# Optimization experiments

Measured on AMD Instinct MI355X. Metric: run time of the kernel, lower is better.

## Reference

```python
import jax, jax.numpy as jnp
import numpy as np

B, S, P, D, H, L, DF, O = 8, 1024, 128, 256, 4, 4, 1024, 10
DH = D // H  # 64
EPS = 1e-5


def get_positional_embeddings(seq_len, d):
    i = np.arange(seq_len, dtype=np.float64)[:, None]
    j = np.arange(d, dtype=np.float64)[None, :]
    even = np.sin(i / 10000 ** (j / d))
    odd = np.cos(i / 10000 ** ((j - 1) / d))
    return jnp.asarray(np.where(j % 2 == 0, even, odd), dtype=jnp.float32)


def layernorm(x, g, b):
    m = jnp.mean(x, axis=-1, keepdims=True)
    v = jnp.mean(jnp.square(x - m), axis=-1, keepdims=True)
    return (x - m) * jax.lax.rsqrt(v + EPS) * g + b


def setup_inputs() -> dict:
    key = jax.random.key(0)
    ks = jax.random.split(key, 20)
    w = lambda k, shp: (jax.random.normal(k, shp, dtype=jnp.float32) * 0.02)
    return {
        "images": jax.random.normal(ks[0], (B, S, P), dtype=jnp.float32),
        "Wp": w(ks[1], (D, P)), "bp": jnp.zeros((D,), jnp.float32),
        "cls": jax.random.uniform(ks[2], (1, D), dtype=jnp.float32),
        "pos": get_positional_embeddings(S + 1, D),
        "ln1_g": jnp.ones((L, D), jnp.float32), "ln1_b": jnp.zeros((L, D), jnp.float32),
        "Wq": w(ks[3], (L, H, DH, DH)), "bq": jnp.zeros((L, H, DH), jnp.float32),
        "Wk": w(ks[4], (L, H, DH, DH)), "bk": jnp.zeros((L, H, DH), jnp.float32),
        "Wv": w(ks[5], (L, H, DH, DH)), "bv": jnp.zeros((L, H, DH), jnp.float32),
        "ln2_g": jnp.ones((L, D), jnp.float32), "ln2_b": jnp.zeros((L, D), jnp.float32),
        "W1": w(ks[6], (L, DF, D)), "b1": jnp.zeros((L, DF), jnp.float32),
        "W2": w(ks[7], (L, D, DF)), "b2": jnp.zeros((L, D), jnp.float32),
        "Wo": w(ks[8], (O, D)), "bo": jnp.zeros((O,), jnp.float32),
    }


def msa(x, Wq, bq, Wk, bk, Wv, bv):
    b, s, _ = x.shape
    xh = x.reshape(b, s, H, DH)  # split heads along feature dim
    # torch Linear: y = x @ W.T + b, per head
    q = jnp.einsum("bshd,hed->bhse", xh, Wq) + bq[None, :, None, :]
    k = jnp.einsum("bshd,hed->bhse", xh, Wk) + bk[None, :, None, :]
    v = jnp.einsum("bshd,hed->bhse", xh, Wv) + bv[None, :, None, :]
    scores = jnp.einsum("bhqd,bhkd->bhqk", q, k) / (DH ** 0.5)
    attn = jax.nn.softmax(scores, axis=-1)
    out = jnp.einsum("bhqk,bhkd->bhqd", attn, v)  # [b,h,s,dh]
    return out.transpose(0, 2, 1, 3).reshape(b, s, D)  # hstack heads


def reference(images, Wp, bp, cls, pos, ln1_g, ln1_b, Wq, bq, Wk, bk, Wv, bv,
              ln2_g, ln2_b, W1, b1, W2, b2, Wo, bo):
    tokens = jnp.einsum("bsp,dp->bsd", images, Wp) + bp
    x = jnp.concatenate([jnp.broadcast_to(cls[None], (B, 1, D)), tokens], axis=1)
    x = x + pos[None]
    for l in range(L):
        x = x + msa(layernorm(x, ln1_g[l], ln1_b[l]), Wq[l], bq[l], Wk[l], bk[l], Wv[l], bv[l])
        h = layernorm(x, ln2_g[l], ln2_b[l])
        h = jax.nn.gelu(jnp.einsum("bsd,fd->bsf", h, W1[l]) + b1[l], approximate=False)
        x = x + jnp.einsum("bsf,df->bsd", h, W2[l]) + b2[l]
    logits = x[:, 0] @ Wo.T + bo
    return jax.nn.softmax(logits, axis=-1)
```

## Files before the change

kernel.cpp:

```cpp
#include <hip/hip_runtime.h>
#include <hip/hip_bf16.h>
#include <cmath>

constexpr int B  = 8;
constexpr int S  = 1024;
constexpr int P  = 128;
constexpr int D  = 256;
constexpr int H  = 4;
constexpr int L  = 4;
constexpr int DF = 1024;
constexpr int O  = 10;
constexpr int DH = D / H;
constexpr int SP = S + 1;
constexpr int N  = B * SP;
constexpr int KVPAD = 1088;

typedef short bf16x8 __attribute__((ext_vector_type(8)));
typedef float f32x4 __attribute__((ext_vector_type(4)));
typedef float f32x16 __attribute__((ext_vector_type(16)));
typedef unsigned int u32;
typedef unsigned short u16;

static __device__ __forceinline__ u16 f2b(float f) {
    __hip_bfloat16 h = __float2bfloat16(f);
    u16 u; __builtin_memcpy(&u, &h, 2);
    return u;
}
static __device__ __forceinline__ float b2f(u16 u) {
    u32 uu = (u32)u << 16; float f; __builtin_memcpy(&f, &uu, 4);
    return f;
}
static __device__ __forceinline__ u32 pk2(float a, float b) {
    return (u32)f2b(a) | ((u32)f2b(b) << 16);
}
static __device__ __forceinline__ void gload_lds16(const void* g, void* l) {
    __builtin_amdgcn_global_load_lds((const __attribute__((address_space(1))) unsigned int*)g,
                                     (__attribute__((address_space(3))) unsigned int*)l, 16, 0, 0);
}

__global__ void cvt_all(const float* __restrict__ s0, u16* __restrict__ d0, int n0,
                        const float* __restrict__ s1, u16* __restrict__ d1, int n1,
                        const float* __restrict__ s2, u16* __restrict__ d2, int n2,
                        const float* __restrict__ s3, u16* __restrict__ d3, int n3) {
    int y = blockIdx.y;
    const float* s = y == 0 ? s0 : y == 1 ? s1 : y == 2 ? s2 : s3;
    u16* d = y == 0 ? d0 : y == 1 ? d1 : y == 2 ? d2 : d3;
    int n = y == 0 ? n0 : y == 1 ? n1 : y == 2 ? n2 : n3;
    int i = blockIdx.x * 256 + threadIdx.x;
    if (i < n) {
        float4 v = ((const float4*)s)[i];
        ushort4 o;
        o.x = f2b(v.x); o.y = f2b(v.y); o.z = f2b(v.z); o.w = f2b(v.w);
        ((ushort4*)d)[i] = o;
    }
}

__global__ void cls_kernel(const float* __restrict__ cls, const float* __restrict__ pos,
                           float* __restrict__ x) {
    int b = blockIdx.x, t = threadIdx.x;
    x[(size_t)b * SP * D + t] = cls[t] + pos[t];
}

__global__ void build_wqkv(const float* __restrict__ Wq, const float* __restrict__ bq,
                           const float* __restrict__ Wk, const float* __restrict__ bk,
                           const float* __restrict__ Wv, const float* __restrict__ bv,
                           u16* __restrict__ Wout, float* __restrict__ bout) {
    int r = blockIdx.x, l = blockIdx.y, c = threadIdx.x;
    int sec = r >> 8;
    int ef = r & 255, h = ef >> 6, e = ef & 63;
    const float* W  = sec == 0 ? Wq : sec == 1 ? Wk : Wv;
    const float* bi = sec == 0 ? bq : sec == 1 ? bk : bv;
    float scale = sec == 0 ? 0.125f * 1.4426950408889634f : 1.0f;
    float val = ((c >> 6) == h) ? W[(((size_t)l * H + h) * 64 + e) * 64 + (c & 63)] * scale : 0.f;
    Wout[((size_t)l * 768 + r) * 256 + c] = f2b(val);
    if (c == 0) bout[(size_t)l * 768 + r] = bi[((size_t)l * H + h) * 64 + e] * scale;
}

template <int EPI>
__global__ __launch_bounds__(256) void gemm_bf16(
        const u16* __restrict__ X, const u16* __restrict__ W,
        const float* __restrict__ bias, const float* __restrict__ pos,
        float* __restrict__ Yf, u16* __restrict__ Yb,
        int M, int F, int K, int kLen) {
    __shared__ u16 Al[2][64 * 64];
    __shared__ u16 Bl[2][128 * 64];
    const int t = threadIdx.x;
    const int m0 = blockIdx.y * 64, f0 = blockIdx.x * 128;
    const int w = t >> 6, l = t & 63;
    const int wm = w >> 1, wn = w & 1;
    const int q = l & 15, g = l >> 4;
    const int kOff = blockIdx.z * kLen;
    const int lr8 = l >> 3, lp = l & 7;

    f32x4 acc[2][4];
    const f32x4 zz = {0.f, 0.f, 0.f, 0.f};
#pragma unroll
    for (int i = 0; i < 2; ++i)
#pragma unroll
        for (int j = 0; j < 4; ++j) acc[i][j] = zz;

    auto stage = [&](int sb, int kbase) {
#pragma unroll
        for (int i = 0; i < 2; ++i) {
            int ca = w + 4 * i;
            int row = ca * 8 + lr8;
            int j = lp ^ (row & 7);
            gload_lds16(X + (size_t)(m0 + row) * K + kbase + j * 8, &Al[sb][ca * 512]);
        }
#pragma unroll
        for (int i = 0; i < 4; ++i) {
            int cb = w + 4 * i;
            int row = cb * 8 + lr8;
            int j = lp ^ (row & 7);
            gload_lds16(W + (size_t)(f0 + row) * K + kbase + j * 8, &Bl[sb][cb * 512]);
        }
    };

    const int nt = kLen / 64;
    stage(0, kOff);
    __syncthreads();
    int sb = 0;
    for (int ts = 0; ts < nt; ++ts) {
        if (ts + 1 < nt) stage(sb ^ 1, kOff + (ts + 1) * 64);
#pragma unroll
        for (int kk = 0; kk < 2; ++kk) {
            bf16x8 a[2], bfr[4];
#pragma unroll
            for (int fi = 0; fi < 2; ++fi) {
                int row = wm * 32 + fi * 16 + q;
                a[fi] = *(const bf16x8*)&Al[sb][row * 64 + (((kk * 4 + g) ^ (row & 7)) * 8)];
            }
#pragma unroll
            for (int fj = 0; fj < 4; ++fj) {
                int row = wn * 64 + fj * 16 + q;
                bfr[fj] = *(const bf16x8*)&Bl[sb][row * 64 + (((kk * 4 + g) ^ (row & 7)) * 8)];
            }
#pragma unroll
            for (int fi = 0; fi < 2; ++fi)
#pragma unroll
                for (int fj = 0; fj < 4; ++fj)
                    acc[fi][fj] = __builtin_amdgcn_mfma_f32_16x16x32_bf16(a[fi], bfr[fj], acc[fi][fj], 0, 0, 0);
        }
        __syncthreads();
        sb ^= 1;
    }

#pragma unroll
    for (int fi = 0; fi < 2; ++fi) {
#pragma unroll
        for (int r = 0; r < 4; ++r) {
            int m = m0 + wm * 32 + fi * 16 + g * 4 + r;
            if (m >= M) continue;
#pragma unroll
            for (int fj = 0; fj < 4; ++fj) {
                int f = f0 + wn * 64 + fj * 16 + q;
                float val = acc[fi][fj][r];
                if constexpr (EPI == 0) {
                    val += bias[f];
                    int s = m & 1023, bb = m >> 10;
                    size_t n = (size_t)bb * SP + s + 1;
                    Yf[n * D + f] = val + pos[(size_t)(s + 1) * D + f];
                } else if constexpr (EPI == 1) {
                    val += bias[f];
                    float gel = 0.5f * val * (1.0f + erff(val * 0.70710678118654752f));
                    Yb[(size_t)m * F + f] = f2b(gel);
                } else if constexpr (EPI == 2) {
                    val += bias[f];
                    Yf[(size_t)m * F + f] += val;
                } else if constexpr (EPI == 3) {
                    val += bias[f];
                    Yb[(size_t)m * F + f] = f2b(val);
                } else {
                    (Yf + (size_t)blockIdx.z * M * F)[(size_t)m * F + f] = val;
                }
            }
        }
    }
}

__global__ void transpose_v(const u16* __restrict__ qkv, u16* __restrict__ VTg) {
    __shared__ u16 tile[64][70];
    int bh = blockIdx.y, t0 = blockIdx.x * 64;
    int b = bh >> 2, h = bh & 3;
    int t = threadIdx.x;
    int r = t >> 3, c8 = (t & 7) * 8;
#pragma unroll
    for (int it = 0; it < 2; ++it) {
        int sp = t0 + it * 32 + r; if (sp > S) sp = S;
        uint4 v = *(const uint4*)(qkv + ((size_t)b * SP + sp) * 768 + 512 + h * 64 + c8);
        u32* dst = (u32*)&tile[it * 32 + r][c8];
        const u32* pv = (const u32*)&v;
#pragma unroll
        for (int k = 0; k < 4; ++k) dst[k] = pv[k];
    }
    __syncthreads();
#pragma unroll
    for (int it = 0; it < 2; ++it) {
        int d = it * 32 + (t >> 3);
        int spc = (t & 7) * 8;
        u16 tmp[8];
#pragma unroll
        for (int j = 0; j < 8; ++j) tmp[j] = tile[spc + j][d];
        *(uint4*)(VTg + ((size_t)bh * 64 + d) * KVPAD + t0 + spc) = *(const uint4*)tmp;
    }
}

__global__ void layernorm_bf16(const float* __restrict__ src,
                               const float* __restrict__ gw,
                               const float* __restrict__ bw,
                               u16* __restrict__ dst) {
    int row = blockIdx.x * 4 + (threadIdx.x >> 6);
    int l = threadIdx.x & 63;
    float4 v = *(const float4*)(src + (size_t)row * D + l * 4);
    float s = v.x + v.y + v.z + v.w;
    for (int off = 32; off; off >>= 1) s += __shfl_xor(s, off, 64);
    float mean = s * (1.0f / D);
    float dx0 = v.x - mean, dx1 = v.y - mean, dx2 = v.z - mean, dx3 = v.w - mean;
    float sq = dx0 * dx0 + dx1 * dx1 + dx2 * dx2 + dx3 * dx3;
    for (int off = 32; off; off >>= 1) sq += __shfl_xor(sq, off, 64);
    float rs = rsqrtf(sq * (1.0f / D) + 1e-5f);
    float4 gv = *(const float4*)(gw + l * 4);
    float4 bv = *(const float4*)(bw + l * 4);
    ushort4 o;
    o.x = f2b(dx0 * rs * gv.x + bv.x);
    o.y = f2b(dx1 * rs * gv.y + bv.y);
    o.z = f2b(dx2 * rs * gv.z + bv.z);
    o.w = f2b(dx3 * rs * gv.w + bv.w);
    *(ushort4*)(dst + (size_t)row * D + l * 4) = o;
}

__global__ __launch_bounds__(512, 4) void attn_stage(const u16* __restrict__ qkv,
                                                     const u16* __restrict__ VTg,
                                                     u16* __restrict__ opart,
                                                     float* __restrict__ lsum,
                                                     int nqt) {
    const int qg = blockIdx.x, bh = blockIdx.y, quarter = blockIdx.z;
    const int h4 = bh & 3, b = bh >> 2;
    const int t = threadIdx.x;
    const int wv = t >> 6, l = t & 63;
    const int col = l & 31, hh = l >> 5;

    __shared__ u16 Kl[5 * 64 * 64];
    __shared__ u16 Vl[5 * 64 * 64];

    const int kv_start = quarter * 256;
    const int kv_len = (quarter == 3) ? (SP - 768) : 256;
    const int ntiles = (kv_len + 63) >> 6;

    const int qt = qg * 8 + wv;
    const int q0w = qt * 32;

    bf16x8 qf[4];
    {
        int qr = q0w + col; if (qr > S) qr = S;
        const u16* qp = qkv + ((size_t)b * SP + qr) * 768 + h4 * 64 + hh * 8;
#pragma unroll
        for (int c = 0; c < 4; ++c) qf[c] = *(const bf16x8*)(qp + c * 16);
    }

    {
        const int rloc = wv * 8 + (l >> 3);
        const int j = (l & 7) ^ (((rloc >> 3) ^ rloc) & 7);
        for (int tt = 0; tt < ntiles; ++tt) {
            int krow = kv_start + tt * 64 + rloc; if (krow > S) krow = S;
            gload_lds16(qkv + ((size_t)b * SP + krow) * 768 + 256 + h4 * 64 + j * 8,
                        &Kl[(tt * 8 + wv) * 512]);
            gload_lds16(VTg + ((size_t)bh * 64 + rloc) * KVPAD + kv_start + tt * 64 + j * 8,
                        &Vl[(tt * 8 + wv) * 512]);
        }
    }
    __syncthreads();
    if (qt >= nqt) return;

    const int swA = ((col >> 3) ^ col) & 7;
    const int swB = swA ^ 4;

    f32x16 o0, o1;
#pragma unroll
    for (int r = 0; r < 16; ++r) { o0[r] = 0.f; o1[r] = 0.f; }
    float l_run = 0.f;

    for (int tile = 0; tile < ntiles; ++tile) {
        const int kv0 = tile * 64;
        const u16* Kt = &Kl[tile * 4096];
        const u16* Vt = &Vl[tile * 4096];

        f32x16 s0, s1;
#pragma unroll
        for (int r = 0; r < 16; ++r) { s0[r] = 0.f; s1[r] = 0.f; }
        __builtin_amdgcn_s_setprio(1);
#pragma unroll
        for (int c = 0; c < 4; ++c) {
            bf16x8 k0 = *(const bf16x8*)&Kt[col * 64 + (((2 * c + hh) ^ swA) * 8)];
            bf16x8 k1 = *(const bf16x8*)&Kt[(32 + col) * 64 + (((2 * c + hh) ^ swB) * 8)];
            s0 = __builtin_amdgcn_mfma_f32_32x32x16_bf16(k0, qf[c], s0, 0, 0, 0);
            s1 = __builtin_amdgcn_mfma_f32_32x32x16_bf16(k1, qf[c], s1, 0, 0, 0);
        }
        __builtin_amdgcn_s_setprio(0);

        float p[32];
#pragma unroll
        for (int r = 0; r < 16; ++r) { p[r] = s0[r]; p[16 + r] = s1[r]; }

        if (kv0 + 64 > kv_len) {
#pragma unroll
            for (int kvs = 0; kvs < 2; ++kvs)
#pragma unroll
                for (int r = 0; r < 16; ++r) {
                    int kvloc = kvs * 32 + (r & 3) + 8 * (r >> 2) + 4 * hh;
                    if (kv0 + kvloc >= kv_len) p[kvs * 16 + r] = -1e30f;
                }
        }

#pragma unroll
        for (int j = 0; j < 32; ++j) p[j] = exp2f(p[j]);
        {
            float t16[16];
#pragma unroll
            for (int j = 0; j < 16; ++j) t16[j] = p[2 * j] + p[2 * j + 1];
#pragma unroll
            for (int j = 0; j < 8; ++j) t16[j] = t16[j] + t16[j + 8];
#pragma unroll
            for (int j = 0; j < 4; ++j) t16[j] = t16[j] + t16[j + 4];
            l_run += (t16[0] + t16[1]) + (t16[2] + t16[3]);
        }

        __builtin_amdgcn_s_setprio(1);
#pragma unroll
        for (int kvs = 0; kvs < 2; ++kvs) {
            u32 pk[8];
#pragma unroll
            for (int i = 0; i < 8; ++i) pk[i] = pk2(p[kvs * 16 + 2 * i], p[kvs * 16 + 2 * i + 1]);
            u32 ex[4];
#pragma unroll
            for (int kk = 0; kk < 4; ++kk) {
                const int k = (kk < 2) ? kk : kk + 2;
                u32 send = hh ? pk[k] : pk[k + 2];
                ex[kk] = (u32)__shfl_xor((int)send, 32);
            }
#pragma unroll
            for (int cc = 0; cc < 2; ++cc) {
                union { u32 u[4]; bf16x8 v; } pa;
                u32 e0 = ex[cc * 2], e1 = ex[cc * 2 + 1];
                pa.u[0] = hh ? e0 : pk[4 * cc];
                pa.u[1] = hh ? e1 : pk[4 * cc + 1];
                pa.u[2] = hh ? pk[4 * cc + 2] : e0;
                pa.u[3] = hh ? pk[4 * cc + 3] : e1;
                int lch = kvs * 4 + cc * 2 + hh;
                bf16x8 v0 = *(const bf16x8*)&Vt[col * 64 + ((lch ^ swA) * 8)];
                bf16x8 v1 = *(const bf16x8*)&Vt[(32 + col) * 64 + ((lch ^ swB) * 8)];
                o0 = __builtin_amdgcn_mfma_f32_32x32x16_bf16(pa.v, v0, o0, 0, 0, 0);
                o1 = __builtin_amdgcn_mfma_f32_32x32x16_bf16(pa.v, v1, o1, 0, 0, 0);
            }
        }
        __builtin_amdgcn_s_setprio(0);
    }

    float l_full = l_run + __shfl_xor(l_run, 32);
    float inv = 1.0f / l_full;
    const size_t obase = ((size_t)quarter * 32 + bh) * SP;
#pragma unroll
    for (int r = 0; r < 16; ++r) {
        int qrow = (r & 3) + 8 * (r >> 2) + 4 * hh;
        float iv = __shfl(inv, qrow);
        int qq = q0w + qrow;
        if (qq < SP) {
            opart[(obase + qq) * 64 + col]      = f2b(o0[r] * iv);
            opart[(obase + qq) * 64 + 32 + col] = f2b(o1[r] * iv);
        }
    }
    if (l < 32) {
        int qq = q0w + l;
        if (qq < SP) lsum[obase + qq] = l_full;
    }
}

__global__ void combine_ln2(const u16* __restrict__ opart, const float* __restrict__ lsum,
                            const float* __restrict__ gw, const float* __restrict__ bw,
                            float* __restrict__ x, u16* __restrict__ lnb) {
    int row = blockIdx.x * 4 + (threadIdx.x >> 6);
    int l = threadIdx.x & 63;
    int b = row / SP, qq = row % SP;
    int h = l >> 4, d0 = (l * 4) & 63;
    int bh = b * 4 + h;
    float csum = 0.f, a0 = 0.f, a1 = 0.f, a2 = 0.f, a3 = 0.f;
#pragma unroll
    for (int i = 0; i < 4; ++i) {
        size_t idx = ((size_t)i * 32 + bh) * SP + qq;
        float c = lsum[idx];
        csum += c;
        ushort4 ov = *(const ushort4*)&opart[idx * 64 + d0];
        a0 += c * b2f(ov.x); a1 += c * b2f(ov.y); a2 += c * b2f(ov.z); a3 += c * b2f(ov.w);
    }
    float inv = 1.0f / csum;
    float4 xv = *(const float4*)(x + (size_t)row * D + l * 4);
    xv.x += a0 * inv; xv.y += a1 * inv; xv.z += a2 * inv; xv.w += a3 * inv;
    *(float4*)(x + (size_t)row * D + l * 4) = xv;

    float s = xv.x + xv.y + xv.z + xv.w;
    for (int off = 32; off; off >>= 1) s += __shfl_xor(s, off, 64);
    float mean = s * (1.0f / D);
    float dx0 = xv.x - mean, dx1 = xv.y - mean, dx2 = xv.z - mean, dx3 = xv.w - mean;
    float sq = dx0 * dx0 + dx1 * dx1 + dx2 * dx2 + dx3 * dx3;
    for (int off = 32; off; off >>= 1) sq += __shfl_xor(sq, off, 64);
    float rs = rsqrtf(sq * (1.0f / D) + 1e-5f);
    float4 gv = *(const float4*)(gw + l * 4);
    float4 bv = *(const float4*)(bw + l * 4);
    ushort4 o;
    o.x = f2b(dx0 * rs * gv.x + bv.x);
    o.y = f2b(dx1 * rs * gv.y + bv.y);
    o.z = f2b(dx2 * rs * gv.z + bv.z);
    o.w = f2b(dx3 * rs * gv.w + bv.w);
    *(ushort4*)(lnb + (size_t)row * D + l * 4) = o;
}

__global__ void combine2_ln1(const float* __restrict__ Pk, const float* __restrict__ b2,
                             const float* __restrict__ gw, const float* __restrict__ bw,
                             float* __restrict__ x, u16* __restrict__ lnb) {
    int row = blockIdx.x * 4 + (threadIdx.x >> 6);
    int l = threadIdx.x & 63;
    float4 p0 = ((const float4*)Pk)[(size_t)row * 64 + l];
    float4 p1 = ((const float4*)Pk)[(size_t)N * 64 + (size_t)row * 64 + l];
    float4 bv2 = *(const float4*)(b2 + l * 4);
    float4 xv = *(const float4*)(x + (size_t)row * D + l * 4);
    xv.x += p0.x + p1.x + bv2.x;
    xv.y += p0.y + p1.y + bv2.y;
    xv.z += p0.z + p1.z + bv2.z;
    xv.w += p0.w + p1.w + bv2.w;
    *(float4*)(x + (size_t)row * D + l * 4) = xv;

    float s = xv.x + xv.y + xv.z + xv.w;
    for (int off = 32; off; off >>= 1) s += __shfl_xor(s, off, 64);
    float mean = s * (1.0f / D);
    float dx0 = xv.x - mean, dx1 = xv.y - mean, dx2 = xv.z - mean, dx3 = xv.w - mean;
    float sq = dx0 * dx0 + dx1 * dx1 + dx2 * dx2 + dx3 * dx3;
    for (int off = 32; off; off >>= 1) sq += __shfl_xor(sq, off, 64);
    float rs = rsqrtf(sq * (1.0f / D) + 1e-5f);
    float4 gv = *(const float4*)(gw + l * 4);
    float4 bv = *(const float4*)(bw + l * 4);
    ushort4 o;
    o.x = f2b(dx0 * rs * gv.x + bv.x);
    o.y = f2b(dx1 * rs * gv.y + bv.y);
    o.z = f2b(dx2 * rs * gv.z + bv.z);
    o.w = f2b(dx3 * rs * gv.w + bv.w);
    *(ushort4*)(lnb + (size_t)row * D + l * 4) = o;
}

__global__ void combine_cls_ln2(const u16* __restrict__ opart, const float* __restrict__ lsum,
                                const float* __restrict__ x,
                                const float* __restrict__ gw, const float* __restrict__ bw,
                                float* __restrict__ x_cls, u16* __restrict__ lnb_cls) {
    int b = blockIdx.x * 4 + (threadIdx.x >> 6);
    int l = threadIdx.x & 63;
    int h = l >> 4, d0 = (l * 4) & 63;
    int bh = b * 4 + h;
    float csum = 0.f, a0 = 0.f, a1 = 0.f, a2 = 0.f, a3 = 0.f;
#pragma unroll
    for (int i = 0; i < 4; ++i) {
        size_t idx = ((size_t)i * 32 + bh) * SP;
        float c = lsum[idx];
        csum += c;
        ushort4 ov = *(const ushort4*)&opart[idx * 64 + d0];
        a0 += c * b2f(ov.x); a1 += c * b2f(ov.y); a2 += c * b2f(ov.z); a3 += c * b2f(ov.w);
    }
    float inv = 1.0f / csum;
    float4 xv = *(const float4*)(x + (size_t)b * SP * D + l * 4);
    xv.x += a0 * inv; xv.y += a1 * inv; xv.z += a2 * inv; xv.w += a3 * inv;
    *(float4*)(x_cls + (size_t)b * D + l * 4) = xv;

    float s = xv.x + xv.y + xv.z + xv.w;
    for (int off = 32; off; off >>= 1) s += __shfl_xor(s, off, 64);
    float mean = s * (1.0f / D);
    float dx0 = xv.x - mean, dx1 = xv.y - mean, dx2 = xv.z - mean, dx3 = xv.w - mean;
    float sq = dx0 * dx0 + dx1 * dx1 + dx2 * dx2 + dx3 * dx3;
    for (int off = 32; off; off >>= 1) sq += __shfl_xor(sq, off, 64);
    float rs = rsqrtf(sq * (1.0f / D) + 1e-5f);
    float4 gv = *(const float4*)(gw + l * 4);
    float4 bv = *(const float4*)(bw + l * 4);
    ushort4 o;
    o.x = f2b(dx0 * rs * gv.x + bv.x);
    o.y = f2b(dx1 * rs * gv.y + bv.y);
    o.z = f2b(dx2 * rs * gv.z + bv.z);
    o.w = f2b(dx3 * rs * gv.w + bv.w);
    *(ushort4*)(lnb_cls + (size_t)b * D + l * 4) = o;
}

__global__ void head_kernel(const float* __restrict__ xc,
                            const float* __restrict__ Wo,
                            const float* __restrict__ bo,
                            float* __restrict__ out) {
    __shared__ float logits[B][O];
    int t = threadIdx.x;
    if (t < B * O) {
        int b = t / O, o = t % O;
        const float* xr = xc + (size_t)b * D;
        float acc = bo[o];
        for (int d = 0; d < D; ++d) acc += xr[d] * Wo[(size_t)o * D + d];
        logits[b][o] = acc;
    }
    __syncthreads();
    if (t < B) {
        float mx = -1e30f;
        for (int o = 0; o < O; ++o) mx = fmaxf(mx, logits[t][o]);
        float s = 0.f, e[O];
        for (int o = 0; o < O; ++o) { e[o] = expf(logits[t][o] - mx); s += e[o]; }
        float inv = 1.0f / s;
        for (int o = 0; o < O; ++o) out[t * O + o] = e[o] * inv;
    }
}

extern "C" void kernel_launch(void* const* d_in, const int* in_sizes, int n_in,
                              void* d_out, int out_size, void* d_ws, size_t ws_size,
                              hipStream_t stream) {
    const float* images = (const float*)d_in[0];
    const float* Wp     = (const float*)d_in[1];
    const float* bp     = (const float*)d_in[2];
    const float* cls    = (const float*)d_in[3];
    const float* pos    = (const float*)d_in[4];
    const float* ln1_g  = (const float*)d_in[5];
    const float* ln1_b  = (const float*)d_in[6];
    const float* Wq     = (const float*)d_in[7];
    const float* bq     = (const float*)d_in[8];
    const float* Wk     = (const float*)d_in[9];
    const float* bk     = (const float*)d_in[10];
    const float* Wv     = (const float*)d_in[11];
    const float* bv     = (const float*)d_in[12];
    const float* ln2_g  = (const float*)d_in[13];
    const float* ln2_b  = (const float*)d_in[14];
    const float* W1     = (const float*)d_in[15];
    const float* b1     = (const float*)d_in[16];
    const float* W2     = (const float*)d_in[17];
    const float* b2     = (const float*)d_in[18];
    const float* Wo     = (const float*)d_in[19];
    const float* bo     = (const float*)d_in[20];
    float* out = (float*)d_out;

    auto align256 = [](size_t v) { return (v + 255) & ~(size_t)255; };
    char* p = (char*)d_ws;
    float* x      = (float*)p; p += align256((size_t)N * D * 4);
    u16* lnb      = (u16*)p;   p += align256((size_t)N * D * 2);
    u16* qkvbuf   = (u16*)p;   p += align256((size_t)(N + 64) * 768 * 2);
    char* midop   = p;         p += align256((size_t)N * DF * 2);
    float* Pk     = (float*)p; p += align256((size_t)2 * N * D * 4);
    float* lsum   = (float*)p; p += align256((size_t)4 * 32 * SP * 4);
    u16* VTg      = (u16*)p;   p += align256((size_t)32 * 64 * KVPAD * 2);
    u16* imgb     = (u16*)p;   p += align256((size_t)B * S * P * 2);
    u16* Wpb      = (u16*)p;   p += align256((size_t)D * P * 2);
    u16* W1b      = (u16*)p;   p += align256((size_t)L * DF * D * 2);
    u16* W2b      = (u16*)p;   p += align256((size_t)L * D * DF * 2);
    u16* Wqkvb    = (u16*)p;   p += align256((size_t)L * 768 * 256 * 2);
    float* bqkvf  = (float*)p; p += align256((size_t)L * 768 * 4);
    float* x_cls  = (float*)p; p += align256((size_t)64 * D * 4);
    u16* lnb_cls  = (u16*)p;   p += align256((size_t)64 * D * 2);
    u16* mid_cls  = (u16*)p;   p += align256((size_t)64 * DF * 2);
    u16* mid      = (u16*)midop;
    u16* opart    = (u16*)midop;

    cvt_all<<<dim3(1024, 4), 256, 0, stream>>>(
        images, imgb, B * S * P / 4,
        Wp, Wpb, D * P / 4,
        W1, W1b, L * DF * D / 4,
        W2, W2b, L * D * DF / 4);
    build_wqkv<<<dim3(768, L), 256, 0, stream>>>(Wq, bq, Wk, bk, Wv, bv, Wqkvb, bqkvf);

    gemm_bf16<0><<<dim3(2, 128, 1), 256, 0, stream>>>(
        imgb, Wpb, bp, pos, x, nullptr, B * S, D, P, P);
    cls_kernel<<<B, D, 0, stream>>>(cls, pos, x);
    layernorm_bf16<<<N / 4, 256, 0, stream>>>(x, ln1_g, ln1_b, lnb);

    for (int l = 0; l < 3; ++l) {
        gemm_bf16<3><<<dim3(6, 129, 1), 256, 0, stream>>>(
            lnb, Wqkvb + (size_t)l * 768 * 256, bqkvf + (size_t)l * 768,
            nullptr, nullptr, qkvbuf, N, 768, D, D);
        transpose_v<<<dim3(17, 32), 256, 0, stream>>>(qkvbuf, VTg);
        attn_stage<<<dim3(5, 32, 4), 512, 0, stream>>>(qkvbuf, VTg, opart, lsum, 33);
        combine_ln2<<<N / 4, 256, 0, stream>>>(opart, lsum, ln2_g + l * D, ln2_b + l * D, x, lnb);
        gemm_bf16<1><<<dim3(8, 129, 1), 256, 0, stream>>>(
            lnb, W1b + (size_t)l * DF * D, b1 + (size_t)l * DF,
            nullptr, nullptr, mid, N, DF, D, D);
        gemm_bf16<4><<<dim3(2, 129, 2), 256, 0, stream>>>(
            mid, W2b + (size_t)l * D * DF, nullptr, nullptr, Pk, nullptr, N, D, DF, DF / 2);
        combine2_ln1<<<N / 4, 256, 0, stream>>>(Pk, b2 + (size_t)l * D,
                                                ln1_g + (l + 1) * D, ln1_b + (l + 1) * D, x, lnb);
    }

    {
        const int l = 3;
        gemm_bf16<3><<<dim3(6, 129, 1), 256, 0, stream>>>(
            lnb, Wqkvb + (size_t)l * 768 * 256, bqkvf + (size_t)l * 768,
            nullptr, nullptr, qkvbuf, N, 768, D, D);
        transpose_v<<<dim3(17, 32), 256, 0, stream>>>(qkvbuf, VTg);
        attn_stage<<<dim3(1, 32, 4), 512, 0, stream>>>(qkvbuf, VTg, opart, lsum, 1);
        combine_cls_ln2<<<2, 256, 0, stream>>>(opart, lsum, x, ln2_g + l * D, ln2_b + l * D,
                                               x_cls, lnb_cls);
        gemm_bf16<1><<<dim3(8, 1, 1), 256, 0, stream>>>(
            lnb_cls, W1b + (size_t)l * DF * D, b1 + (size_t)l * DF,
            nullptr, nullptr, mid_cls, B, DF, D, D);
        gemm_bf16<2><<<dim3(2, 1, 1), 256, 0, stream>>>(
            mid_cls, W2b + (size_t)l * D * DF, b2 + (size_t)l * D,
            nullptr, x_cls, nullptr, B, D, DF, DF);
    }

    head_kernel<<<1, 256, 0, stream>>>(x_cls, Wo, bo, out);
}
```

Baseline: 357.5 us.

## Fuse final-layer tail, drop attention normalization pass, store split-K partials as bf16

The separate cls-token and first-layernorm kernels are merged, and the last-layer tail (combine, LN2, MLP, head and softmax for the CLS rows) is collapsed into one per-batch kernel, removing about five small launches. Attention partials are no longer normalized per quarter, so the combine step simply sums them and divides by the total lsum. The split-K W2 partial outputs are written in bf16 instead of fp32, halving that intermediate traffic. In exchange, partials are rounded to bf16 before summing, and unnormalized attention outputs may lose a little precision.

```diff
diff --git a/kernel.cpp b/kernel.cpp
--- a/kernel.cpp
+++ b/kernel.cpp
@@ -53,12 +53,6 @@
         o.x = f2b(v.x); o.y = f2b(v.y); o.z = f2b(v.z); o.w = f2b(v.w);
         ((ushort4*)d)[i] = o;
     }
-}
-
-__global__ void cls_kernel(const float* __restrict__ cls, const float* __restrict__ pos,
-                           float* __restrict__ x) {
-    int b = blockIdx.x, t = threadIdx.x;
-    x[(size_t)b * SP * D + t] = cls[t] + pos[t];
 }
 
 __global__ void build_wqkv(const float* __restrict__ Wq, const float* __restrict__ bq,
@@ -164,14 +158,11 @@
                     val += bias[f];
                     float gel = 0.5f * val * (1.0f + erff(val * 0.70710678118654752f));
                     Yb[(size_t)m * F + f] = f2b(gel);
-                } else if constexpr (EPI == 2) {
-                    val += bias[f];
-                    Yf[(size_t)m * F + f] += val;
                 } else if constexpr (EPI == 3) {
                     val += bias[f];
                     Yb[(size_t)m * F + f] = f2b(val);
                 } else {
-                    (Yf + (size_t)blockIdx.z * M * F)[(size_t)m * F + f] = val;
+                    Yb[(size_t)blockIdx.z * M * F + (size_t)m * F + f] = f2b(val);
                 }
             }
         }
@@ -205,13 +196,20 @@
     }
 }
 
-__global__ void layernorm_bf16(const float* __restrict__ src,
-                               const float* __restrict__ gw,
-                               const float* __restrict__ bw,
-                               u16* __restrict__ dst) {
+__global__ void ln_first(const float* __restrict__ cls, const float* __restrict__ pos,
+                         const float* __restrict__ gw, const float* __restrict__ bw,
+                         float* __restrict__ x, u16* __restrict__ dst) {
     int row = blockIdx.x * 4 + (threadIdx.x >> 6);
     int l = threadIdx.x & 63;
-    float4 v = *(const float4*)(src + (size_t)row * D + l * 4);
+    float4 v;
+    if ((row % SP) == 0) {
+        float4 c = *(const float4*)(cls + l * 4);
+        float4 pp = *(const float4*)(pos + l * 4);
+        v.x = c.x + pp.x; v.y = c.y + pp.y; v.z = c.z + pp.z; v.w = c.w + pp.w;
+        *(float4*)(x + (size_t)row * D + l * 4) = v;
+    } else {
+        v = *(const float4*)(x + (size_t)row * D + l * 4);
+    }
     float s = v.x + v.y + v.z + v.w;
     for (int off = 32; off; off >>= 1) s += __shfl_xor(s, off, 64);
     float mean = s * (1.0f / D);
@@ -357,16 +355,14 @@
     }
 
     float l_full = l_run + __shfl_xor(l_run, 32);
-    float inv = 1.0f / l_full;
     const size_t obase = ((size_t)quarter * 32 + bh) * SP;
 #pragma unroll
     for (int r = 0; r < 16; ++r) {
         int qrow = (r & 3) + 8 * (r >> 2) + 4 * hh;
-        float iv = __shfl(inv, qrow);
         int qq = q0w + qrow;
         if (qq < SP) {
-            opart[(obase + qq) * 64 + col]      = f2b(o0[r] * iv);
-            opart[(obase + qq) * 64 + 32 + col] = f2b(o1[r] * iv);
+            opart[(obase + qq) * 64 + col]      = f2b(o0[r]);
+            opart[(obase + qq) * 64 + 32 + col] = f2b(o1[r]);
         }
     }
     if (l < 32) {
@@ -387,10 +383,9 @@
 #pragma unroll
     for (int i = 0; i < 4; ++i) {
         size_t idx = ((size_t)i * 32 + bh) * SP + qq;
-        float c = lsum[idx];
-        csum += c;
+        csum += lsum[idx];
         ushort4 ov = *(const ushort4*)&opart[idx * 64 + d0];
-        a0 += c * b2f(ov.x); a1 += c * b2f(ov.y); a2 += c * b2f(ov.z); a3 += c * b2f(ov.w);
+        a0 += b2f(ov.x); a1 += b2f(ov.y); a2 += b2f(ov.z); a3 += b2f(ov.w);
     }
     float inv = 1.0f / csum;
     float4 xv = *(const float4*)(x + (size_t)row * D + l * 4);
@@ -414,19 +409,19 @@
     *(ushort4*)(lnb + (size_t)row * D + l * 4) = o;
 }
 
-__global__ void combine2_ln1(const float* __restrict__ Pk, const float* __restrict__ b2,
+__global__ void combine2_ln1(const u16* __restrict__ Pkb, const float* __restrict__ b2,
                              const float* __restrict__ gw, const float* __restrict__ bw,
                              float* __restrict__ x, u16* __restrict__ lnb) {
     int row = blockIdx.x * 4 + (threadIdx.x >> 6);
     int l = threadIdx.x & 63;
-    float4 p0 = ((const float4*)Pk)[(size_t)row * 64 + l];
-    float4 p1 = ((const float4*)Pk)[(size_t)N * 64 + (size_t)row * 64 + l];
+    ushort4 p0 = *(const ushort4*)(Pkb + (size_t)row * D + l * 4);
+    ushort4 p1 = *(const ushort4*)(Pkb + (size_t)N * D + (size_t)row * D + l * 4);
     float4 bv2 = *(const float4*)(b2 + l * 4);
     float4 xv = *(const float4*)(x + (size_t)row * D + l * 4);
-    xv.x += p0.x + p1.x + bv2.x;
-    xv.y += p0.y + p1.y + bv2.y;
-    xv.z += p0.z + p1.z + bv2.z;
-    xv.w += p0.w + p1.w + bv2.w;
+    xv.x += b2f(p0.x) + b2f(p1.x) + bv2.x;
+    xv.y += b2f(p0.y) + b2f(p1.y) + bv2.y;
+    xv.z += b2f(p0.z) + b2f(p1.z) + bv2.z;
+    xv.w += b2f(p0.w) + b2f(p1.w) + bv2.w;
     *(float4*)(x + (size_t)row * D + l * 4) = xv;
 
     float s = xv.x + xv.y + xv.z + xv.w;
@@ -446,66 +441,88 @@
     *(ushort4*)(lnb + (size_t)row * D + l * 4) = o;
 }
 
-__global__ void combine_cls_ln2(const u16* __restrict__ opart, const float* __restrict__ lsum,
-                                const float* __restrict__ x,
-                                const float* __restrict__ gw, const float* __restrict__ bw,
-                                float* __restrict__ x_cls, u16* __restrict__ lnb_cls) {
-    int b = blockIdx.x * 4 + (threadIdx.x >> 6);
-    int l = threadIdx.x & 63;
-    int h = l >> 4, d0 = (l * 4) & 63;
-    int bh = b * 4 + h;
-    float csum = 0.f, a0 = 0.f, a1 = 0.f, a2 = 0.f, a3 = 0.f;
+__global__ void tail_fused(const u16* __restrict__ opart, const float* __restrict__ lsum,
+                           const float* __restrict__ x,
+                           const float* __restrict__ g2, const float* __restrict__ b2w,
+                           const u16* __restrict__ W1l, const float* __restrict__ b1l,
+                           const u16* __restrict__ W2l, const float* __restrict__ b2l,
+                           const float* __restrict__ Wo, const float* __restrict__ bo,
+                           float* __restrict__ out) {
+    __shared__ float ln[256];
+    __shared__ float hbuf[1024];
+    __shared__ float xc[256];
+    __shared__ float red[4];
+    __shared__ float logits[O];
+    const int b = blockIdx.x, t = threadIdx.x;
+    const int h = t >> 6, dl = t & 63;
+
+    float csum = 0.f, a = 0.f;
 #pragma unroll
     for (int i = 0; i < 4; ++i) {
-        size_t idx = ((size_t)i * 32 + bh) * SP;
-        float c = lsum[idx];
-        csum += c;
-        ushort4 ov = *(const ushort4*)&opart[idx * 64 + d0];
-        a0 += c * b2f(ov.x); a1 += c * b2f(ov.y); a2 += c * b2f(ov.z); a3 += c * b2f(ov.w);
-    }
-    float inv = 1.0f / csum;
-    float4 xv = *(const float4*)(x + (size_t)b * SP * D + l * 4);
-    xv.x += a0 * inv; xv.y += a1 * inv; xv.z += a2 * inv; xv.w += a3 * inv;
-    *(float4*)(x_cls + (size_t)b * D + l * 4) = xv;
-
-    float s = xv.x + xv.y + xv.z + xv.w;
+        size_t idx = ((size_t)i * 32 + b * 4 + h) * SP;
+        csum += lsum[idx];
+        a += b2f(opart[idx * 64 + dl]);
+    }
+    float xv = x[(size_t)b * SP * D + t] + a / csum;
+    xc[t] = xv;
+
+    float s = xv;
     for (int off = 32; off; off >>= 1) s += __shfl_xor(s, off, 64);
-    float mean = s * (1.0f / D);
-    float dx0 = xv.x - mean, dx1 = xv.y - mean, dx2 = xv.z - mean, dx3 = xv.w - mean;
-    float sq = dx0 * dx0 + dx1 * dx1 + dx2 * dx2 + dx3 * dx3;
+    if ((t & 63) == 0) red[t >> 6] = s;
+    __syncthreads();
+    float mean = (red[0] + red[1] + red[2] + red[3]) * (1.0f / D);
+    float dx = xv - mean;
+    float sq = dx * dx;
     for (int off = 32; off; off >>= 1) sq += __shfl_xor(sq, off, 64);
-    float rs = rsqrtf(sq * (1.0f / D) + 1e-5f);
-    float4 gv = *(const float4*)(gw + l * 4);
-    float4 bv = *(const float4*)(bw + l * 4);
-    ushort4 o;
-    o.x = f2b(dx0 * rs * gv.x + bv.x);
-    o.y = f2b(dx1 * rs * gv.y + bv.y);
-    o.z = f2b(dx2 * rs * gv.z + bv.z);
-    o.w = f2b(dx3 * rs * gv.w + bv.w);
-    *(ushort4*)(lnb_cls + (size_t)b * D + l * 4) = o;
-}
-
-__global__ void head_kernel(const float* __restrict__ xc,
-                            const float* __restrict__ Wo,
-                            const float* __restrict__ bo,
-                            float* __restrict__ out) {
-    __shared__ float logits[B][O];
-    int t = threadIdx.x;
-    if (t < B * O) {
-        int b = t / O, o = t % O;
-        const float* xr = xc + (size_t)b * D;
-        float acc = bo[o];
-        for (int d = 0; d < D; ++d) acc += xr[d] * Wo[(size_t)o * D + d];
-        logits[b][o] = acc;
-    }
-    __syncthreads();
-    if (t < B) {
-        float mx = -1e30f;
-        for (int o = 0; o < O; ++o) mx = fmaxf(mx, logits[t][o]);
-        float s = 0.f, e[O];
-        for (int o = 0; o < O; ++o) { e[o] = expf(logits[t][o] - mx); s += e[o]; }
-        float inv = 1.0f / s;
-        for (int o = 0; o < O; ++o) out[t * O + o] = e[o] * inv;
+    __syncthreads();
+    if ((t & 63) == 0) red[t >> 6] = sq;
+    __syncthreads();
+    float var = (red[0] + red[1] + red[2] + red[3]) * (1.0f / D);
+    ln[t] = dx * rsqrtf(var + 1e-5f) * g2[t] + b2w[t];
+    __syncthreads();
+
+#pragma unroll
+    for (int i = 0; i < 4; ++i) {
+        int f = t + i * 256;
+        const u16* wr = W1l + (size_t)f * D;
+        float acc = b1l[f];
+        for (int d = 0; d < D; d += 8) {
+            bf16x8 wv = *(const bf16x8*)(wr + d);
+            const u16* wu = (const u16*)&wv;
+#pragma unroll
+            for (int j = 0; j < 8; ++j) acc += ln[d + j] * b2f(wu[j]);
+        }
+        hbuf[f] = 0.5f * acc * (1.0f + erff(acc * 0.70710678118654752f));
+    }
+    __syncthreads();
+
+    {
+        const u16* wr = W2l + (size_t)t * DF;
+        float acc = b2l[t];
+        for (int f = 0; f < DF; f += 8) {
+            bf16x8 wv = *(const bf16x8*)(wr + f);
+            const u16* wu = (const u16*)&wv;
+#pragma unroll
+            for (int j = 0; j < 8; ++j) acc += hbuf[f + j] * b2f(wu[j]);
+        }
+        xc[t] += acc;
+    }
+    __syncthreads();
+
+    if (t < O) {
+        float acc = bo[t];
+        const float* wr = Wo + (size_t)t * D;
+        for (int d = 0; d < D; ++d) acc += xc[d] * wr[d];
+        logits[t] = acc;
+    }
+    __syncthreads();
+    if (t == 0) {
+        float mx = logits[0];
+        for (int o = 1; o < O; ++o) mx = fmaxf(mx, logits[o]);
+        float ssum = 0.f, e[O];
+        for (int o = 0; o < O; ++o) { e[o] = expf(logits[o] - mx); ssum += e[o]; }
+        float inv = 1.0f / ssum;
+        for (int o = 0; o < O; ++o) out[b * O + o] = e[o] * inv;
     }
 }
 
@@ -539,9 +556,9 @@
     char* p = (char*)d_ws;
     float* x      = (float*)p; p += align256((size_t)N * D * 4);
     u16* lnb      = (u16*)p;   p += align256((size_t)N * D * 2);
-    u16* qkvbuf   = (u16*)p;   p += align256((size_t)(N + 64) * 768 * 2);
+    u16* qkvbuf   = (u16*)p;   p += align256((size_t)(N + 128) * 768 * 2);
     char* midop   = p;         p += align256((size_t)N * DF * 2);
-    float* Pk     = (float*)p; p += align256((size_t)2 * N * D * 4);
+    u16* Pkb      = (u16*)p;   p += align256((size_t)2 * N * D * 2);
     float* lsum   = (float*)p; p += align256((size_t)4 * 32 * SP * 4);
     u16* VTg      = (u16*)p;   p += align256((size_t)32 * 64 * KVPAD * 2);
     u16* imgb     = (u16*)p;   p += align256((size_t)B * S * P * 2);
@@ -550,9 +567,6 @@
     u16* W2b      = (u16*)p;   p += align256((size_t)L * D * DF * 2);
     u16* Wqkvb    = (u16*)p;   p += align256((size_t)L * 768 * 256 * 2);
     float* bqkvf  = (float*)p; p += align256((size_t)L * 768 * 4);
-    float* x_cls  = (float*)p; p += align256((size_t)64 * D * 4);
-    u16* lnb_cls  = (u16*)p;   p += align256((size_t)64 * D * 2);
-    u16* mid_cls  = (u16*)p;   p += align256((size_t)64 * DF * 2);
     u16* mid      = (u16*)midop;
     u16* opart    = (u16*)midop;
 
@@ -565,8 +579,7 @@
 
     gemm_bf16<0><<<dim3(2, 128, 1), 256, 0, stream>>>(
         imgb, Wpb, bp, pos, x, nullptr, B * S, D, P, P);
-    cls_kernel<<<B, D, 0, stream>>>(cls, pos, x);
-    layernorm_bf16<<<N / 4, 256, 0, stream>>>(x, ln1_g, ln1_b, lnb);
+    ln_first<<<N / 4, 256, 0, stream>>>(cls, pos, ln1_g, ln1_b, x, lnb);
 
     for (int l = 0; l < 3; ++l) {
         gemm_bf16<3><<<dim3(6, 129, 1), 256, 0, stream>>>(
@@ -579,8 +592,8 @@
             lnb, W1b + (size_t)l * DF * D, b1 + (size_t)l * DF,
             nullptr, nullptr, mid, N, DF, D, D);
         gemm_bf16<4><<<dim3(2, 129, 2), 256, 0, stream>>>(
-            mid, W2b + (size_t)l * D * DF, nullptr, nullptr, Pk, nullptr, N, D, DF, DF / 2);
-        combine2_ln1<<<N / 4, 256, 0, stream>>>(Pk, b2 + (size_t)l * D,
+            mid, W2b + (size_t)l * D * DF, nullptr, nullptr, nullptr, Pkb, N, D, DF, DF / 2);
+        combine2_ln1<<<N / 4, 256, 0, stream>>>(Pkb, b2 + (size_t)l * D,
                                                 ln1_g + (l + 1) * D, ln1_b + (l + 1) * D, x, lnb);
     }
 
@@ -591,15 +604,10 @@
             nullptr, nullptr, qkvbuf, N, 768, D, D);
         transpose_v<<<dim3(17, 32), 256, 0, stream>>>(qkvbuf, VTg);
         attn_stage<<<dim3(1, 32, 4), 512, 0, stream>>>(qkvbuf, VTg, opart, lsum, 1);
-        combine_cls_ln2<<<2, 256, 0, stream>>>(opart, lsum, x, ln2_g + l * D, ln2_b + l * D,
-                                               x_cls, lnb_cls);
-        gemm_bf16<1><<<dim3(8, 1, 1), 256, 0, stream>>>(
-            lnb_cls, W1b + (size_t)l * DF * D, b1 + (size_t)l * DF,
-            nullptr, nullptr, mid_cls, B, DF, D, D);
-        gemm_bf16<2><<<dim3(2, 1, 1), 256, 0, stream>>>(
-            mid_cls, W2b + (size_t)l * D * DF, b2 + (size_t)l * D,
-            nullptr, x_cls, nullptr, B, D, DF, DF);
-    }
-
-    head_kernel<<<1, 256, 0, stream>>>(x_cls, Wo, bo, out);
-}
+        tail_fused<<<B, 256, 0, stream>>>(opart, lsum, x,
+                                          ln2_g + l * D, ln2_b + l * D,
+                                          W1b + (size_t)l * DF * D, b1 + (size_t)l * DF,
+                                          W2b + (size_t)l * D * DF, b2 + (size_t)l * D,
+                                          Wo, bo, out);
+    }
+}
```

After: 359.4 us. Within noise of the previous version (+0.5%).
